# Kernel tuning notes

Hardware: AMD Instinct MI355X
Metric: run time of the kernel (lower is better)

## Reference

```python
import jax, jax.numpy as jnp
import numpy as np

E4M3 = jnp.float8_e4m3fn  # HPU e4m3 (max 240) approximated by e4m3fn grid
E5M2 = jnp.float8_e5m2


def fp8_quant_dequant(x, scale, dt):
    # cast_to_fp8(x, scale) followed by inline dequant (1/scale) inside fp8_gemm_v2
    return (x * scale).astype(dt).astype(jnp.float32) / scale


def setup_inputs() -> dict:
    key = jax.random.key(0)
    k1, k2 = jax.random.split(key)
    A, B, C, OUT = 4, 2048, 2048, 8192
    return {
        "input": jax.random.normal(k1, (A, B, C), jnp.float32),
        "weight": jax.random.normal(k2, (OUT, C), jnp.float32) * 0.02,
        "input_scale_e4m3": jnp.ones((), jnp.float32),
        "weight_scale_e4m3": jnp.ones((), jnp.float32),
        "input_scale_e5m2": jnp.ones((), jnp.float32),
        "weight_scale_e5m2": jnp.ones((), jnp.float32),
        "grad_scale_e5m2": jnp.ones((), jnp.float32),
    }


def reference(input, weight, input_scale_e4m3, weight_scale_e4m3,
              input_scale_e5m2, weight_scale_e5m2, grad_scale_e5m2):
    A, B, C = input.shape
    x2d = input.reshape(A * B, C)
    # forward path uses the e4m3 copies from cast_to_fp8_hybrid
    x_q = fp8_quant_dequant(x2d, input_scale_e4m3, E4M3)      # [A*B, C]
    w_q = fp8_quant_dequant(weight, weight_scale_e4m3, E4M3)  # [OUT, C]
    out = x_q @ w_q.T                                          # [A*B, OUT]
    return out.reshape(A, B, -1)
```

## Files before the change

### kernel.cpp

```cpp
#include <hip/hip_runtime.h>

typedef float floatx16 __attribute__((ext_vector_type(16)));
typedef int   intx4    __attribute__((ext_vector_type(4)));
typedef int   intx8    __attribute__((ext_vector_type(8)));

#define GEMM_M 8192
#define GEMM_N 8192
#define GEMM_K 2048
#define NT     32

__global__ __launch_bounds__(256) void quant_e4m3(const float* __restrict__ x,
                                                  const float* __restrict__ scale,
                                                  int* __restrict__ q)
{
    const float s = scale[0];
    const int base = blockIdx.x * 1024 + threadIdx.x;
    const float4* __restrict__ x4 = (const float4*)x;
#pragma unroll
    for (int j = 0; j < 4; ++j) {
        float4 v = x4[base + j * 256];
        int p;
        p = __builtin_amdgcn_cvt_pk_fp8_f32(v.x * s, v.y * s, 0, false);
        p = __builtin_amdgcn_cvt_pk_fp8_f32(v.z * s, v.w * s, p, true);
        q[base + j * 256] = p;
    }
}

#define GLDS(gp, lp) __builtin_amdgcn_global_load_lds( \
    (const __attribute__((address_space(1))) void*)(gp), \
    (__attribute__((address_space(3))) void*)(lp), 16, 0, 0)

#define MFMA1(A_, B_, C_) __builtin_amdgcn_mfma_scale_f32_32x32x64_f8f6f4( \
    (A_), (B_), (C_), 0, 0, 0, 0x7f7f7f7f, 0, 0x7f7f7f7f)

__global__ __launch_bounds__(512, 2) void gemm_fp8_mx(
    const unsigned char* __restrict__ Aq,
    const unsigned char* __restrict__ Bq,
    float* __restrict__ C,
    const float* __restrict__ sa,
    const float* __restrict__ sb)
{
    extern __shared__ __align__(16) unsigned char lds[];
    unsigned char* ldsA = lds;
    unsigned char* ldsB = lds + 65536;

    const int tid  = threadIdx.x;
    const int lane = tid & 63;
    const int wave = tid >> 6;
    const int wm   = wave >> 2;
    const int wn   = wave & 3;

    const int bid = blockIdx.x;
    const int xcd = bid & 7;
    const int idx = bid >> 3;
    const int bm  = xcd * 4 + ((idx & 15) >> 2);
    const int bn  = (idx >> 4) * 4 + (idx & 3);

    const int srow   = tid >> 2;
    const int schunk = ((tid & 3) ^ ((tid >> 3) & 3)) << 4;
    const unsigned char* gA0 = Aq + (size_t)(bm * 256 +       srow) * GEMM_K + schunk;
    const unsigned char* gA1 = Aq + (size_t)(bm * 256 + 128 + srow) * GEMM_K + schunk;
    const unsigned char* gB0 = Bq + (size_t)(bn * 256 +       srow) * GEMM_K + schunk;
    const unsigned char* gB1 = Bq + (size_t)(bn * 256 + 128 + srow) * GEMM_K + schunk;
    const int l0 = tid * 16;

    const int mloc = lane & 31;
    const int h    = lane >> 5;
    const int swz  = (mloc >> 1) & 3;
    const int aoff_lo = (wm * 128 + mloc) * 64 + (((2 * h)     ^ swz) << 4);
    const int aoff_hi = (wm * 128 + mloc) * 64 + (((2 * h + 1) ^ swz) << 4);
    const int boff_lo = (wn * 64  + mloc) * 64 + (((2 * h)     ^ swz) << 4);
    const int boff_hi = (wn * 64  + mloc) * 64 + (((2 * h + 1) ^ swz) << 4);

    floatx16 acc[4][2];
#pragma unroll
    for (int i = 0; i < 4; ++i)
#pragma unroll
        for (int j = 0; j < 2; ++j)
            acc[i][j] = (floatx16)(0.0f);

    intx8 af0, af1, bf0, bf1;

#define LDFRAG(dst, base, olo, ohi) do { \
    intx4 _lo = *(const intx4*)((base) + (olo)); \
    intx4 _hi = *(const intx4*)((base) + (ohi)); \
    (dst) = __builtin_shufflevector(_lo, _hi, 0, 1, 2, 3, 4, 5, 6, 7); \
} while (0)

#define STAGE_A(KT) do { \
    const int _b = (KT) & 3; const size_t _ko = (size_t)(KT) * 64; \
    GLDS(gA0 + _ko, ldsA + _b * 16384 +        l0); \
    GLDS(gA1 + _ko, ldsA + _b * 16384 + 8192 + l0); \
} while (0)

#define STAGE_B(KT) do { \
    const int _b = (KT) & 3; const size_t _ko = (size_t)(KT) * 64; \
    GLDS(gB0 + _ko, ldsB + _b * 16384 +        l0); \
    GLDS(gB1 + _ko, ldsB + _b * 16384 + 8192 + l0); \
} while (0)

#define P0(KT, STAGE_STMT) do { \
    const unsigned char* _bA = ldsA + ((KT) & 3) * 16384; \
    const unsigned char* _bB = ldsB + ((KT) & 3) * 16384; \
    LDFRAG(af0, _bA, aoff_lo,        aoff_hi); \
    LDFRAG(af1, _bA, aoff_lo + 2048, aoff_hi + 2048); \
    LDFRAG(bf0, _bB, boff_lo,        boff_hi); \
    LDFRAG(bf1, _bB, boff_lo + 2048, boff_hi + 2048); \
    STAGE_STMT; \
    __builtin_amdgcn_s_barrier(); \
    asm volatile("s_waitcnt lgkmcnt(0)" ::: "memory"); \
    __builtin_amdgcn_s_setprio(1); \
    acc[0][0] = MFMA1(af0, bf0, acc[0][0]); \
    acc[0][1] = MFMA1(af0, bf1, acc[0][1]); \
    acc[1][0] = MFMA1(af1, bf0, acc[1][0]); \
    acc[1][1] = MFMA1(af1, bf1, acc[1][1]); \
    __builtin_amdgcn_s_setprio(0); \
    __builtin_amdgcn_s_barrier(); \
} while (0)

#define P1(KT, STAGE_STMT, TAILWAIT) do { \
    const unsigned char* _bA = ldsA + ((KT) & 3) * 16384; \
    LDFRAG(af0, _bA, aoff_lo + 4096, aoff_hi + 4096); \
    LDFRAG(af1, _bA, aoff_lo + 6144, aoff_hi + 6144); \
    STAGE_STMT; \
    __builtin_amdgcn_s_barrier(); \
    asm volatile("s_waitcnt lgkmcnt(0)" ::: "memory"); \
    __builtin_amdgcn_s_setprio(1); \
    acc[2][0] = MFMA1(af0, bf0, acc[2][0]); \
    acc[2][1] = MFMA1(af0, bf1, acc[2][1]); \
    acc[3][0] = MFMA1(af1, bf0, acc[3][0]); \
    acc[3][1] = MFMA1(af1, bf1, acc[3][1]); \
    __builtin_amdgcn_s_setprio(0); \
    TAILWAIT; \
    __builtin_amdgcn_s_barrier(); \
} while (0)

    STAGE_A(0); STAGE_B(0);
    STAGE_A(1); STAGE_B(1);
    STAGE_A(2); STAGE_B(2);
    asm volatile("s_waitcnt vmcnt(8)" ::: "memory");
    __builtin_amdgcn_s_barrier();

#pragma unroll 1
    for (int kt = 0; kt <= NT - 4; ++kt) {
        P0(kt, STAGE_A(kt + 3));
        P1(kt, STAGE_B(kt + 3),
           asm volatile("s_waitcnt vmcnt(8)" ::: "memory"));
    }
    P0(NT - 3, (void)0);
    P1(NT - 3, (void)0, asm volatile("s_waitcnt vmcnt(4)" ::: "memory"));
    P0(NT - 2, (void)0);
    P1(NT - 2, (void)0, asm volatile("s_waitcnt vmcnt(0)" ::: "memory"));
    P0(NT - 1, (void)0);
    P1(NT - 1, (void)0, (void)0);

    const float inv = 1.0f / (sa[0] * sb[0]);
#pragma unroll
    for (int ti = 0; ti < 4; ++ti) {
        const int row0 = bm * 256 + wm * 128 + ti * 32 + 4 * h;
#pragma unroll
        for (int tj = 0; tj < 2; ++tj) {
            const int col = bn * 256 + wn * 64 + tj * 32 + mloc;
#pragma unroll
            for (int reg = 0; reg < 16; ++reg) {
                const int row = row0 + (reg & 3) + 8 * (reg >> 2);
                C[(size_t)row * GEMM_N + col] = acc[ti][tj][reg] * inv;
            }
        }
    }
}

extern "C" void kernel_launch(void* const* d_in, const int* in_sizes, int n_in,
                              void* d_out, int out_size, void* d_ws, size_t ws_size,
                              hipStream_t stream) {
    const float* x    = (const float*)d_in[0];
    const float* w    = (const float*)d_in[1];
    const float* s_in = (const float*)d_in[2];
    const float* s_w  = (const float*)d_in[3];
    float* out = (float*)d_out;

    unsigned char* qx = (unsigned char*)d_ws;
    unsigned char* qw = qx + (size_t)GEMM_M * GEMM_K;

    quant_e4m3<<<in_sizes[0] / 4096, 256, 0, stream>>>(x, s_in, (int*)qx);
    quant_e4m3<<<in_sizes[1] / 4096, 256, 0, stream>>>(w, s_w, (int*)qw);

    static int attr_done = 0;
    if (!attr_done) {
        hipFuncSetAttribute((const void*)gemm_fp8_mx,
                            hipFuncAttributeMaxDynamicSharedMemorySize, 131072);
        attr_done = 1;
    }
    gemm_fp8_mx<<<dim3(1024), dim3(512), 131072, stream>>>(qx, qw, out, s_in, s_w);
}
```

Baseline: 478.2 us.

## Use 4 waves per block with 128x128 per-wave tiles in FP8 GEMM

Halves the workgroup to 256 threads (4 waves in a 2x2 grid), so each wave computes a 128x128 sub-tile with a 4x4 accumulator array instead of 128x64. Each thread now issues four global-to-LDS loads per operand per stage, and the vmcnt waits are adjusted to match. This raises MFMA work per LDS fragment load and halves the number of waves hitting barriers. In exchange it roughly doubles accumulator register pressure (256 VGPRs of accumulators), limits occupancy to one block per CU given 128KB LDS, and leaves fewer waves to hide latency.

```diff
diff --git a/kernel.cpp b/kernel.cpp
--- a/kernel.cpp
+++ b/kernel.cpp
@@ -33,7 +33,7 @@
 #define MFMA1(A_, B_, C_) __builtin_amdgcn_mfma_scale_f32_32x32x64_f8f6f4( \
     (A_), (B_), (C_), 0, 0, 0, 0x7f7f7f7f, 0, 0x7f7f7f7f)
 
-__global__ __launch_bounds__(512, 2) void gemm_fp8_mx(
+__global__ __launch_bounds__(256, 1) void gemm_fp8_mx(
     const unsigned char* __restrict__ Aq,
     const unsigned char* __restrict__ Bq,
     float* __restrict__ C,
@@ -47,8 +47,8 @@
     const int tid  = threadIdx.x;
     const int lane = tid & 63;
     const int wave = tid >> 6;
-    const int wm   = wave >> 2;
-    const int wn   = wave & 3;
+    const int wm   = wave >> 1;
+    const int wn   = wave & 1;
 
     const int bid = blockIdx.x;
     const int xcd = bid & 7;
@@ -58,28 +58,26 @@
 
     const int srow   = tid >> 2;
     const int schunk = ((tid & 3) ^ ((tid >> 3) & 3)) << 4;
-    const unsigned char* gA0 = Aq + (size_t)(bm * 256 +       srow) * GEMM_K + schunk;
-    const unsigned char* gA1 = Aq + (size_t)(bm * 256 + 128 + srow) * GEMM_K + schunk;
-    const unsigned char* gB0 = Bq + (size_t)(bn * 256 +       srow) * GEMM_K + schunk;
-    const unsigned char* gB1 = Bq + (size_t)(bn * 256 + 128 + srow) * GEMM_K + schunk;
+    const unsigned char* gA = Aq + (size_t)(bm * 256 + srow) * GEMM_K + schunk;
+    const unsigned char* gB = Bq + (size_t)(bn * 256 + srow) * GEMM_K + schunk;
     const int l0 = tid * 16;
 
     const int mloc = lane & 31;
     const int h    = lane >> 5;
     const int swz  = (mloc >> 1) & 3;
-    const int aoff_lo = (wm * 128 + mloc) * 64 + (((2 * h)     ^ swz) << 4);
-    const int aoff_hi = (wm * 128 + mloc) * 64 + (((2 * h + 1) ^ swz) << 4);
-    const int boff_lo = (wn * 64  + mloc) * 64 + (((2 * h)     ^ swz) << 4);
-    const int boff_hi = (wn * 64  + mloc) * 64 + (((2 * h + 1) ^ swz) << 4);
-
-    floatx16 acc[4][2];
+    const int alo = (wm * 128 + mloc) * 64 + (((2 * h)     ^ swz) << 4);
+    const int ahi = (wm * 128 + mloc) * 64 + (((2 * h + 1) ^ swz) << 4);
+    const int blo = (wn * 128 + mloc) * 64 + (((2 * h)     ^ swz) << 4);
+    const int bhi = (wn * 128 + mloc) * 64 + (((2 * h + 1) ^ swz) << 4);
+
+    floatx16 acc[4][4];
 #pragma unroll
     for (int i = 0; i < 4; ++i)
 #pragma unroll
-        for (int j = 0; j < 2; ++j)
+        for (int j = 0; j < 4; ++j)
             acc[i][j] = (floatx16)(0.0f);
 
-    intx8 af0, af1, bf0, bf1;
+    intx8 af0, af1, bf0, bf1, bf2, bf3;
 
 #define LDFRAG(dst, base, olo, ohi) do { \
     intx4 _lo = *(const intx4*)((base) + (olo)); \
@@ -89,47 +87,61 @@
 
 #define STAGE_A(KT) do { \
     const int _b = (KT) & 3; const size_t _ko = (size_t)(KT) * 64; \
-    GLDS(gA0 + _ko, ldsA + _b * 16384 +        l0); \
-    GLDS(gA1 + _ko, ldsA + _b * 16384 + 8192 + l0); \
+    GLDS(gA + _ko,                     ldsA + _b * 16384 +         l0); \
+    GLDS(gA + _ko +     64 * GEMM_K,   ldsA + _b * 16384 +  4096 + l0); \
+    GLDS(gA + _ko + 2 * 64 * GEMM_K,   ldsA + _b * 16384 +  8192 + l0); \
+    GLDS(gA + _ko + 3 * 64 * GEMM_K,   ldsA + _b * 16384 + 12288 + l0); \
 } while (0)
 
 #define STAGE_B(KT) do { \
     const int _b = (KT) & 3; const size_t _ko = (size_t)(KT) * 64; \
-    GLDS(gB0 + _ko, ldsB + _b * 16384 +        l0); \
-    GLDS(gB1 + _ko, ldsB + _b * 16384 + 8192 + l0); \
+    GLDS(gB + _ko,                     ldsB + _b * 16384 +         l0); \
+    GLDS(gB + _ko +     64 * GEMM_K,   ldsB + _b * 16384 +  4096 + l0); \
+    GLDS(gB + _ko + 2 * 64 * GEMM_K,   ldsB + _b * 16384 +  8192 + l0); \
+    GLDS(gB + _ko + 3 * 64 * GEMM_K,   ldsB + _b * 16384 + 12288 + l0); \
 } while (0)
 
 #define P0(KT, STAGE_STMT) do { \
     const unsigned char* _bA = ldsA + ((KT) & 3) * 16384; \
     const unsigned char* _bB = ldsB + ((KT) & 3) * 16384; \
-    LDFRAG(af0, _bA, aoff_lo,        aoff_hi); \
-    LDFRAG(af1, _bA, aoff_lo + 2048, aoff_hi + 2048); \
-    LDFRAG(bf0, _bB, boff_lo,        boff_hi); \
-    LDFRAG(bf1, _bB, boff_lo + 2048, boff_hi + 2048); \
+    LDFRAG(af0, _bA, alo,        ahi); \
+    LDFRAG(af1, _bA, alo + 2048, ahi + 2048); \
+    LDFRAG(bf0, _bB, blo,        bhi); \
+    LDFRAG(bf1, _bB, blo + 2048, bhi + 2048); \
+    LDFRAG(bf2, _bB, blo + 4096, bhi + 4096); \
+    LDFRAG(bf3, _bB, blo + 6144, bhi + 6144); \
     STAGE_STMT; \
     __builtin_amdgcn_s_barrier(); \
     asm volatile("s_waitcnt lgkmcnt(0)" ::: "memory"); \
     __builtin_amdgcn_s_setprio(1); \
     acc[0][0] = MFMA1(af0, bf0, acc[0][0]); \
     acc[0][1] = MFMA1(af0, bf1, acc[0][1]); \
+    acc[0][2] = MFMA1(af0, bf2, acc[0][2]); \
+    acc[0][3] = MFMA1(af0, bf3, acc[0][3]); \
     acc[1][0] = MFMA1(af1, bf0, acc[1][0]); \
     acc[1][1] = MFMA1(af1, bf1, acc[1][1]); \
+    acc[1][2] = MFMA1(af1, bf2, acc[1][2]); \
+    acc[1][3] = MFMA1(af1, bf3, acc[1][3]); \
     __builtin_amdgcn_s_setprio(0); \
     __builtin_amdgcn_s_barrier(); \
 } while (0)
 
 #define P1(KT, STAGE_STMT, TAILWAIT) do { \
     const unsigned char* _bA = ldsA + ((KT) & 3) * 16384; \
-    LDFRAG(af0, _bA, aoff_lo + 4096, aoff_hi + 4096); \
-    LDFRAG(af1, _bA, aoff_lo + 6144, aoff_hi + 6144); \
+    LDFRAG(af0, _bA, alo + 4096, ahi + 4096); \
+    LDFRAG(af1, _bA, alo + 6144, ahi + 6144); \
     STAGE_STMT; \
     __builtin_amdgcn_s_barrier(); \
     asm volatile("s_waitcnt lgkmcnt(0)" ::: "memory"); \
     __builtin_amdgcn_s_setprio(1); \
     acc[2][0] = MFMA1(af0, bf0, acc[2][0]); \
     acc[2][1] = MFMA1(af0, bf1, acc[2][1]); \
+    acc[2][2] = MFMA1(af0, bf2, acc[2][2]); \
+    acc[2][3] = MFMA1(af0, bf3, acc[2][3]); \
     acc[3][0] = MFMA1(af1, bf0, acc[3][0]); \
     acc[3][1] = MFMA1(af1, bf1, acc[3][1]); \
+    acc[3][2] = MFMA1(af1, bf2, acc[3][2]); \
+    acc[3][3] = MFMA1(af1, bf3, acc[3][3]); \
     __builtin_amdgcn_s_setprio(0); \
     TAILWAIT; \
     __builtin_amdgcn_s_barrier(); \
@@ -138,17 +150,17 @@
     STAGE_A(0); STAGE_B(0);
     STAGE_A(1); STAGE_B(1);
     STAGE_A(2); STAGE_B(2);
-    asm volatile("s_waitcnt vmcnt(8)" ::: "memory");
+    asm volatile("s_waitcnt vmcnt(16)" ::: "memory");
     __builtin_amdgcn_s_barrier();
 
 #pragma unroll 1
     for (int kt = 0; kt <= NT - 4; ++kt) {
         P0(kt, STAGE_A(kt + 3));
         P1(kt, STAGE_B(kt + 3),
-           asm volatile("s_waitcnt vmcnt(8)" ::: "memory"));
+           asm volatile("s_waitcnt vmcnt(16)" ::: "memory"));
     }
     P0(NT - 3, (void)0);
-    P1(NT - 3, (void)0, asm volatile("s_waitcnt vmcnt(4)" ::: "memory"));
+    P1(NT - 3, (void)0, asm volatile("s_waitcnt vmcnt(8)" ::: "memory"));
     P0(NT - 2, (void)0);
     P1(NT - 2, (void)0, asm volatile("s_waitcnt vmcnt(0)" ::: "memory"));
     P0(NT - 1, (void)0);
@@ -159,8 +171,8 @@
     for (int ti = 0; ti < 4; ++ti) {
         const int row0 = bm * 256 + wm * 128 + ti * 32 + 4 * h;
 #pragma unroll
-        for (int tj = 0; tj < 2; ++tj) {
-            const int col = bn * 256 + wn * 64 + tj * 32 + mloc;
+        for (int tj = 0; tj < 4; ++tj) {
+            const int col = bn * 256 + wn * 128 + tj * 32 + mloc;
 #pragma unroll
             for (int reg = 0; reg < 16; ++reg) {
                 const int row = row0 + (reg & 3) + 8 * (reg >> 2);
@@ -191,5 +203,5 @@
                             hipFuncAttributeMaxDynamicSharedMemorySize, 131072);
         attr_done = 1;
     }
-    gemm_fp8_mx<<<dim3(1024), dim3(512), 131072, stream>>>(qx, qw, out, s_in, s_w);
+    gemm_fp8_mx<<<dim3(1024), dim3(256), 131072, stream>>>(qx, qw, out, s_in, s_w);
 }
```

After: 475.1 us. About the same (-0.7%).

## Merge half k-steps into one step with a single workgroup barrier

Applied to the files above, without the earlier changes.

The two half-steps per k-tile (P0/P1) become one KSTEP. All A and B fragments are loaded from LDS up front into two extra A fragment registers, and both global-to-LDS stages are issued in the same step. This drops three of the four s_barrier calls and the explicit lgkmcnt waits per k-tile, using sched_barrier fences to keep the instruction order. The cost is more live fragment registers on top of an already large accumulator set, which risks register pressure or spills, and the compiler must now place the LDS waits itself.

```diff
diff --git a/kernel.cpp b/kernel.cpp
--- a/kernel.cpp
+++ b/kernel.cpp
@@ -33,6 +33,8 @@
 #define MFMA1(A_, B_, C_) __builtin_amdgcn_mfma_scale_f32_32x32x64_f8f6f4( \
     (A_), (B_), (C_), 0, 0, 0, 0x7f7f7f7f, 0, 0x7f7f7f7f)
 
+#define SBAR() __builtin_amdgcn_sched_barrier(0)
+
 __global__ __launch_bounds__(512, 2) void gemm_fp8_mx(
     const unsigned char* __restrict__ Aq,
     const unsigned char* __restrict__ Bq,
@@ -67,10 +69,10 @@
     const int mloc = lane & 31;
     const int h    = lane >> 5;
     const int swz  = (mloc >> 1) & 3;
-    const int aoff_lo = (wm * 128 + mloc) * 64 + (((2 * h)     ^ swz) << 4);
-    const int aoff_hi = (wm * 128 + mloc) * 64 + (((2 * h + 1) ^ swz) << 4);
-    const int boff_lo = (wn * 64  + mloc) * 64 + (((2 * h)     ^ swz) << 4);
-    const int boff_hi = (wn * 64  + mloc) * 64 + (((2 * h + 1) ^ swz) << 4);
+    const int alo = (wm * 128 + mloc) * 64 + (((2 * h)     ^ swz) << 4);
+    const int ahi = (wm * 128 + mloc) * 64 + (((2 * h + 1) ^ swz) << 4);
+    const int blo = (wn * 64  + mloc) * 64 + (((2 * h)     ^ swz) << 4);
+    const int bhi = (wn * 64  + mloc) * 64 + (((2 * h + 1) ^ swz) << 4);
 
     floatx16 acc[4][2];
 #pragma unroll
@@ -79,7 +81,7 @@
         for (int j = 0; j < 2; ++j)
             acc[i][j] = (floatx16)(0.0f);
 
-    intx8 af0, af1, bf0, bf1;
+    intx8 af0, af1, af2, af3, bf0, bf1;
 
 #define LDFRAG(dst, base, olo, ohi) do { \
     intx4 _lo = *(const intx4*)((base) + (olo)); \
@@ -99,38 +101,33 @@
     GLDS(gB1 + _ko, ldsB + _b * 16384 + 8192 + l0); \
 } while (0)
 
-#define P0(KT, STAGE_STMT) do { \
+#define KSTEP(KT, SA_STMT, SB_STMT, TAILWAIT) do { \
     const unsigned char* _bA = ldsA + ((KT) & 3) * 16384; \
     const unsigned char* _bB = ldsB + ((KT) & 3) * 16384; \
-    LDFRAG(af0, _bA, aoff_lo,        aoff_hi); \
-    LDFRAG(af1, _bA, aoff_lo + 2048, aoff_hi + 2048); \
-    LDFRAG(bf0, _bB, boff_lo,        boff_hi); \
-    LDFRAG(bf1, _bB, boff_lo + 2048, boff_hi + 2048); \
-    STAGE_STMT; \
-    __builtin_amdgcn_s_barrier(); \
-    asm volatile("s_waitcnt lgkmcnt(0)" ::: "memory"); \
+    LDFRAG(af0, _bA, alo,        ahi); \
+    LDFRAG(af1, _bA, alo + 2048, ahi + 2048); \
+    LDFRAG(bf0, _bB, blo,        bhi); \
+    LDFRAG(bf1, _bB, blo + 2048, bhi + 2048); \
+    SA_STMT; \
+    SBAR(); \
+    LDFRAG(af2, _bA, alo + 4096, ahi + 4096); \
+    LDFRAG(af3, _bA, alo + 6144, ahi + 6144); \
+    SB_STMT; \
+    SBAR(); \
     __builtin_amdgcn_s_setprio(1); \
     acc[0][0] = MFMA1(af0, bf0, acc[0][0]); \
     acc[0][1] = MFMA1(af0, bf1, acc[0][1]); \
     acc[1][0] = MFMA1(af1, bf0, acc[1][0]); \
     acc[1][1] = MFMA1(af1, bf1, acc[1][1]); \
     __builtin_amdgcn_s_setprio(0); \
-    __builtin_amdgcn_s_barrier(); \
-} while (0)
-
-#define P1(KT, STAGE_STMT, TAILWAIT) do { \
-    const unsigned char* _bA = ldsA + ((KT) & 3) * 16384; \
-    LDFRAG(af0, _bA, aoff_lo + 4096, aoff_hi + 4096); \
-    LDFRAG(af1, _bA, aoff_lo + 6144, aoff_hi + 6144); \
-    STAGE_STMT; \
-    __builtin_amdgcn_s_barrier(); \
-    asm volatile("s_waitcnt lgkmcnt(0)" ::: "memory"); \
+    SBAR(); \
     __builtin_amdgcn_s_setprio(1); \
-    acc[2][0] = MFMA1(af0, bf0, acc[2][0]); \
-    acc[2][1] = MFMA1(af0, bf1, acc[2][1]); \
-    acc[3][0] = MFMA1(af1, bf0, acc[3][0]); \
-    acc[3][1] = MFMA1(af1, bf1, acc[3][1]); \
+    acc[2][0] = MFMA1(af2, bf0, acc[2][0]); \
+    acc[2][1] = MFMA1(af2, bf1, acc[2][1]); \
+    acc[3][0] = MFMA1(af3, bf0, acc[3][0]); \
+    acc[3][1] = MFMA1(af3, bf1, acc[3][1]); \
     __builtin_amdgcn_s_setprio(0); \
+    SBAR(); \
     TAILWAIT; \
     __builtin_amdgcn_s_barrier(); \
 } while (0)
@@ -143,16 +140,14 @@
 
 #pragma unroll 1
     for (int kt = 0; kt <= NT - 4; ++kt) {
-        P0(kt, STAGE_A(kt + 3));
-        P1(kt, STAGE_B(kt + 3),
-           asm volatile("s_waitcnt vmcnt(8)" ::: "memory"));
+        KSTEP(kt, STAGE_A(kt + 3), STAGE_B(kt + 3),
+              asm volatile("s_waitcnt vmcnt(8)" ::: "memory"));
     }
-    P0(NT - 3, (void)0);
-    P1(NT - 3, (void)0, asm volatile("s_waitcnt vmcnt(4)" ::: "memory"));
-    P0(NT - 2, (void)0);
-    P1(NT - 2, (void)0, asm volatile("s_waitcnt vmcnt(0)" ::: "memory"));
-    P0(NT - 1, (void)0);
-    P1(NT - 1, (void)0, (void)0);
+    KSTEP(NT - 3, (void)0, (void)0,
+          asm volatile("s_waitcnt vmcnt(4)" ::: "memory"));
+    KSTEP(NT - 2, (void)0, (void)0,
+          asm volatile("s_waitcnt vmcnt(0)" ::: "memory"));
+    KSTEP(NT - 1, (void)0, (void)0, (void)0);
 
     const float inv = 1.0f / (sa[0] * sb[0]);
 #pragma unroll
```

New measurement: 471.0 us. About the same (-1.5%).
